# Kernel tuning notes

Hardware: AMD Instinct MI355X
Metric: run time of the kernel (lower is better)

## Reference

```python
import jax, jax.numpy as jnp
import numpy as np

RANK = 16
ALPHA = 32
SCALING = ALPHA / RANK  # 2.0


def setup_inputs() -> dict:
    key = jax.random.key(0)
    k1, k2, k3 = jax.random.split(key, 3)
    B_, S, D, O = 2, 4096, 4096, 4096
    x = jax.random.normal(k1, (B_, S, D), dtype=jnp.float32)
    # Dequantized base weight, torch Linear layout [out, in]
    W_base = jax.random.normal(k2, (O, D), dtype=jnp.float32) * 0.02
    # kaiming_uniform-ish init for lora_A [rank, in]
    bound = float(np.sqrt(6.0 / (1 + 5) / D))
    A = jax.random.uniform(k3, (RANK, D), dtype=jnp.float32, minval=-bound, maxval=bound)
    # lora_B initialized to zeros [out, rank]
    Bm = jnp.zeros((O, RANK), dtype=jnp.float32)
    return {"x": x, "W_base": W_base, "A": A, "B": Bm}


def reference(x, W_base, A, B):
    # Y = x @ W_base^T + (x @ A^T) @ B^T * scaling   (dropout p=0 -> identity)
    base_out = jnp.einsum('bsd,od->bso', x, W_base)
    lora_mid = jnp.einsum('bsd,rd->bsr', x, A)        # [B,S,rank]
    lora_out = jnp.einsum('bsr,or->bso', lora_mid, B) # [B,S,out]
    return base_out + lora_out * SCALING
```

## Files before the change

### kernel.cpp

```cpp
#include <hip/hip_runtime.h>
#include <hip/hip_bf16.h>

typedef __attribute__((ext_vector_type(8)))  __bf16 bf16x8;
typedef __attribute__((ext_vector_type(4)))  float  f32x4;

__global__ __launch_bounds__(256) void preproc(
    const float* __restrict__ x, const float* __restrict__ A,
    const float* __restrict__ Wf,
    float* __restrict__ mid, __bf16* __restrict__ Xb, __bf16* __restrict__ Wbb,
    int K, int M, long nW8, int wBlocks)
{
    int tid = threadIdx.x;
    if ((int)blockIdx.x < wBlocks) {
        long i = (long)blockIdx.x * 256 + tid;
        long stride = (long)wBlocks * 256;
        for (; i < nW8; i += stride) {
            const f32x4* p = (const f32x4*)(Wf + i * 8);
            f32x4 a = p[0], b = p[1];
            bf16x8 o;
            o[0] = (__bf16)a[0]; o[1] = (__bf16)a[1];
            o[2] = (__bf16)a[2]; o[3] = (__bf16)a[3];
            o[4] = (__bf16)b[0]; o[5] = (__bf16)b[1];
            o[6] = (__bf16)b[2]; o[7] = (__bf16)b[3];
            *(bf16x8*)(Wbb + i * 8) = o;
        }
        return;
    }

    int m0 = ((int)blockIdx.x - wBlocks) * 4;
    float acc[4][16];
#pragma unroll
    for (int row = 0; row < 4; ++row)
#pragma unroll
        for (int r = 0; r < 16; ++r) acc[row][r] = 0.f;

    int iters = K / 2048;
    for (int it = 0; it < iters; ++it) {
        int k = it * 2048 + tid * 8;
        f32x4 xv[4][2];
#pragma unroll
        for (int row = 0; row < 4; ++row) {
            if (m0 + row < M) {
                const float* xr = x + (size_t)(m0 + row) * K;
                xv[row][0] = *(const f32x4*)(xr + k);
                xv[row][1] = *(const f32x4*)(xr + k + 4);
                bf16x8 o;
                o[0] = (__bf16)xv[row][0][0]; o[1] = (__bf16)xv[row][0][1];
                o[2] = (__bf16)xv[row][0][2]; o[3] = (__bf16)xv[row][0][3];
                o[4] = (__bf16)xv[row][1][0]; o[5] = (__bf16)xv[row][1][1];
                o[6] = (__bf16)xv[row][1][2]; o[7] = (__bf16)xv[row][1][3];
                *(bf16x8*)(Xb + (size_t)(m0 + row) * K + k) = o;
            } else {
                f32x4 z = {0.f,0.f,0.f,0.f};
                xv[row][0] = z; xv[row][1] = z;
            }
        }
#pragma unroll
        for (int r = 0; r < 16; ++r) {
            const f32x4* ap = (const f32x4*)(A + (size_t)r * K + k);
            f32x4 a0 = ap[0], a1 = ap[1];
#pragma unroll
            for (int row = 0; row < 4; ++row) {
                acc[row][r] += xv[row][0][0]*a0[0] + xv[row][0][1]*a0[1]
                             + xv[row][0][2]*a0[2] + xv[row][0][3]*a0[3]
                             + xv[row][1][0]*a1[0] + xv[row][1][1]*a1[1]
                             + xv[row][1][2]*a1[2] + xv[row][1][3]*a1[3];
            }
        }
    }

#pragma unroll
    for (int row = 0; row < 4; ++row)
#pragma unroll
        for (int r = 0; r < 16; ++r)
#pragma unroll
            for (int off = 32; off > 0; off >>= 1)
                acc[row][r] += __shfl_down(acc[row][r], off, 64);

    __shared__ float red[4][4][16];
    int lane = tid & 63, w = tid >> 6;
    if (lane == 0) {
#pragma unroll
        for (int row = 0; row < 4; ++row)
#pragma unroll
            for (int r = 0; r < 16; ++r) red[w][row][r] = acc[row][r];
    }
    __syncthreads();
    if (tid < 64) {
        int row = tid >> 4, r = tid & 15;
        if (m0 + row < M) {
            float s = red[0][row][r] + red[1][row][r]
                    + red[2][row][r] + red[3][row][r];
            mid[(size_t)(m0 + row) * 16 + r] = s;
        }
    }
}

__global__ __launch_bounds__(256) void mid_only(
    const float* __restrict__ x, const float* __restrict__ A,
    float* __restrict__ mid, int K, int M)
{
    int tid = threadIdx.x;
    int m0 = blockIdx.x * 4;
    float acc[4][16];
#pragma unroll
    for (int row = 0; row < 4; ++row)
#pragma unroll
        for (int r = 0; r < 16; ++r) acc[row][r] = 0.f;
    int iters = K / 2048;
    for (int it = 0; it < iters; ++it) {
        int k = it * 2048 + tid * 8;
        f32x4 xv[4][2];
#pragma unroll
        for (int row = 0; row < 4; ++row) {
            if (m0 + row < M) {
                const float* xr = x + (size_t)(m0 + row) * K;
                xv[row][0] = *(const f32x4*)(xr + k);
                xv[row][1] = *(const f32x4*)(xr + k + 4);
            } else {
                f32x4 z = {0.f,0.f,0.f,0.f};
                xv[row][0] = z; xv[row][1] = z;
            }
        }
#pragma unroll
        for (int r = 0; r < 16; ++r) {
            const f32x4* ap = (const f32x4*)(A + (size_t)r * K + k);
            f32x4 a0 = ap[0], a1 = ap[1];
#pragma unroll
            for (int row = 0; row < 4; ++row) {
                acc[row][r] += xv[row][0][0]*a0[0] + xv[row][0][1]*a0[1]
                             + xv[row][0][2]*a0[2] + xv[row][0][3]*a0[3]
                             + xv[row][1][0]*a1[0] + xv[row][1][1]*a1[1]
                             + xv[row][1][2]*a1[2] + xv[row][1][3]*a1[3];
            }
        }
    }
#pragma unroll
    for (int row = 0; row < 4; ++row)
#pragma unroll
        for (int r = 0; r < 16; ++r)
#pragma unroll
            for (int off = 32; off > 0; off >>= 1)
                acc[row][r] += __shfl_down(acc[row][r], off, 64);
    __shared__ float red[4][4][16];
    int lane = tid & 63, w = tid >> 6;
    if (lane == 0) {
#pragma unroll
        for (int row = 0; row < 4; ++row)
#pragma unroll
            for (int r = 0; r < 16; ++r) red[w][row][r] = acc[row][r];
    }
    __syncthreads();
    if (tid < 64) {
        int row = tid >> 4, r = tid & 15;
        if (m0 + row < M) {
            float s = red[0][row][r] + red[1][row][r]
                    + red[2][row][r] + red[3][row][r];
            mid[(size_t)(m0 + row) * 16 + r] = s;
        }
    }
}

#define GL16(g, l) __builtin_amdgcn_global_load_lds( \
    (const __attribute__((address_space(1))) void*)(g), \
    (__attribute__((address_space(3))) void*)(l), 16, 0, 0)

#define DSR(dst, addr, IMM) \
    asm volatile("ds_read_b128 %0, %1 offset:" IMM : "=v"(dst) : "v"(addr))

#define BAR()   __builtin_amdgcn_s_barrier()
#define LGKM0() asm volatile("s_waitcnt lgkmcnt(0)" ::: )
#define FENCE() __builtin_amdgcn_sched_barrier(0)
#define VMW(n)  asm volatile("s_waitcnt vmcnt(" #n ")" ::: "memory")

__global__ __launch_bounds__(512, 2) void gemm256(
    const __bf16* __restrict__ Xb,
    const __bf16* __restrict__ Wb,
    const float*  __restrict__ mid,
    const float*  __restrict__ Bl,
    float* __restrict__ out,
    int M, int N, int K)
{
    __shared__ __bf16 As[4][256 * 32];
    __shared__ __bf16 Bs[4][256 * 32];

    const int NT = K >> 5;

    int nbx = N >> 8, nby = M >> 8, nwg = nbx * nby;
    int bid = blockIdx.x, swz = bid;
    if ((nwg & 7) == 0) { int cpx = nwg >> 3; swz = (bid & 7) * cpx + (bid >> 3); }
    int by = swz / nbx, bx = swz % nbx;
    int m0 = by << 8, n0 = bx << 8;

    int tid = threadIdx.x;
    int lane = tid & 63;
    int w = tid >> 6;
    int wm = w >> 2, wn = w & 3;

    int q0 = tid >> 2;
    int c0 = tid & 3;
    int csrc = c0 ^ ((q0 >> 1) & 3);
    const __bf16* sA0 = Xb + (size_t)(m0 + q0) * K + csrc * 8;
    const __bf16* sA1 = sA0 + (size_t)128 * K;
    const __bf16* sB0 = Wb + (size_t)(n0 + q0) * K + csrc * 8;
    const __bf16* sB1 = sB0 + (size_t)128 * K;
    unsigned ldsw = (unsigned)w * 1024;

#define STAGE_A(t, b) do { size_t ko = (size_t)(t) * 32; \
    GL16(sA0 + ko, (char*)As[b] + ldsw); \
    GL16(sA1 + ko, (char*)As[b] + 8192 + ldsw); } while (0)
#define STAGE_B(t, b) do { size_t ko = (size_t)(t) * 32; \
    GL16(sB0 + ko, (char*)Bs[b] + ldsw); \
    GL16(sB1 + ko, (char*)Bs[b] + 8192 + ldsw); } while (0)

    int chunkSwz = (lane >> 4) ^ ((lane >> 1) & 3);
    unsigned aoff = (unsigned)((wm * 128 + (lane & 15)) * 64 + chunkSwz * 16);
    unsigned boff = (unsigned)((wn * 64  + (lane & 15)) * 64 + chunkSwz * 16);
    unsigned a_addr = (unsigned)(size_t)(__attribute__((address_space(3))) __bf16*)&As[0][0] + aoff;
    unsigned b_addr = (unsigned)(size_t)(__attribute__((address_space(3))) __bf16*)&Bs[0][0] + boff;

    f32x4 acc[8][4];
    {
        int kh = lane >> 4;
        bf16x8 bI[4];
#pragma unroll
        for (int j = 0; j < 4; ++j) {
            bf16x8 v = {};
            if (kh < 2) {
                int col = n0 + wn * 64 + j * 16 + (lane & 15);
                const f32x4* p = (const f32x4*)(Bl + (size_t)col * 16 + kh * 8);
                f32x4 v0 = p[0], v1 = p[1];
                v[0] = (__bf16)(2.0f * v0[0]); v[1] = (__bf16)(2.0f * v0[1]);
                v[2] = (__bf16)(2.0f * v0[2]); v[3] = (__bf16)(2.0f * v0[3]);
                v[4] = (__bf16)(2.0f * v1[0]); v[5] = (__bf16)(2.0f * v1[1]);
                v[6] = (__bf16)(2.0f * v1[2]); v[7] = (__bf16)(2.0f * v1[3]);
            }
            bI[j] = v;
        }
#pragma unroll
        for (int i = 0; i < 8; ++i) {
            bf16x8 aI = {};
            if (kh < 2) {
                int row = m0 + wm * 128 + i * 16 + (lane & 15);
                const f32x4* p = (const f32x4*)(mid + (size_t)row * 16 + kh * 8);
                f32x4 v0 = p[0], v1 = p[1];
                aI[0] = (__bf16)v0[0]; aI[1] = (__bf16)v0[1];
                aI[2] = (__bf16)v0[2]; aI[3] = (__bf16)v0[3];
                aI[4] = (__bf16)v1[0]; aI[5] = (__bf16)v1[1];
                aI[6] = (__bf16)v1[2]; aI[7] = (__bf16)v1[3];
            }
            f32x4 z = {0.f, 0.f, 0.f, 0.f};
#pragma unroll
            for (int j = 0; j < 4; ++j)
                acc[i][j] = __builtin_amdgcn_mfma_f32_16x16x32_bf16(aI, bI[j], z, 0, 0, 0);
        }
    }

    STAGE_A(0, 0); STAGE_B(0, 0);
    STAGE_A(1, 1); STAGE_B(1, 1);
    VMW(4);
    BAR();

    bf16x8 af0, af1, af2, af3, af4, af5, af6, af7, bf0, bf1, bf2, bf3;

    for (int t = 0; t < NT; ++t) {
        unsigned aT = a_addr + ((unsigned)(t & 3) << 14);
        unsigned bT = b_addr + ((unsigned)(t & 3) << 14);
        bool p2 = (t + 2) < NT;

        DSR(bf0, bT, "0");    DSR(bf1, bT, "1024");
        DSR(bf2, bT, "2048"); DSR(bf3, bT, "3072");
        DSR(af0, aT, "0");    DSR(af1, aT, "1024");
        DSR(af2, aT, "2048"); DSR(af3, aT, "3072");
        if (p2) STAGE_A(t + 2, (t + 2) & 3);
        BAR();
        LGKM0();
        FENCE();
        __builtin_amdgcn_s_setprio(1);
        acc[0][0] = __builtin_amdgcn_mfma_f32_16x16x32_bf16(af0, bf0, acc[0][0], 0, 0, 0);
        acc[0][1] = __builtin_amdgcn_mfma_f32_16x16x32_bf16(af0, bf1, acc[0][1], 0, 0, 0);
        acc[0][2] = __builtin_amdgcn_mfma_f32_16x16x32_bf16(af0, bf2, acc[0][2], 0, 0, 0);
        acc[0][3] = __builtin_amdgcn_mfma_f32_16x16x32_bf16(af0, bf3, acc[0][3], 0, 0, 0);
        acc[1][0] = __builtin_amdgcn_mfma_f32_16x16x32_bf16(af1, bf0, acc[1][0], 0, 0, 0);
        acc[1][1] = __builtin_amdgcn_mfma_f32_16x16x32_bf16(af1, bf1, acc[1][1], 0, 0, 0);
        acc[1][2] = __builtin_amdgcn_mfma_f32_16x16x32_bf16(af1, bf2, acc[1][2], 0, 0, 0);
        acc[1][3] = __builtin_amdgcn_mfma_f32_16x16x32_bf16(af1, bf3, acc[1][3], 0, 0, 0);
        acc[2][0] = __builtin_amdgcn_mfma_f32_16x16x32_bf16(af2, bf0, acc[2][0], 0, 0, 0);
        acc[2][1] = __builtin_amdgcn_mfma_f32_16x16x32_bf16(af2, bf1, acc[2][1], 0, 0, 0);
        acc[2][2] = __builtin_amdgcn_mfma_f32_16x16x32_bf16(af2, bf2, acc[2][2], 0, 0, 0);
        acc[2][3] = __builtin_amdgcn_mfma_f32_16x16x32_bf16(af2, bf3, acc[2][3], 0, 0, 0);
        acc[3][0] = __builtin_amdgcn_mfma_f32_16x16x32_bf16(af3, bf0, acc[3][0], 0, 0, 0);
        acc[3][1] = __builtin_amdgcn_mfma_f32_16x16x32_bf16(af3, bf1, acc[3][1], 0, 0, 0);
        acc[3][2] = __builtin_amdgcn_mfma_f32_16x16x32_bf16(af3, bf2, acc[3][2], 0, 0, 0);
        acc[3][3] = __builtin_amdgcn_mfma_f32_16x16x32_bf16(af3, bf3, acc[3][3], 0, 0, 0);
        __builtin_amdgcn_s_setprio(0);
        BAR();

        DSR(af4, aT, "4096"); DSR(af5, aT, "5120");
        DSR(af6, aT, "6144"); DSR(af7, aT, "7168");
        if (p2) {
            STAGE_B(t + 2, (t + 2) & 3);
            VMW(4);
        } else {
            VMW(0);
        }
        BAR();
        LGKM0();
        FENCE();
        __builtin_amdgcn_s_setprio(1);
        acc[4][0] = __builtin_amdgcn_mfma_f32_16x16x32_bf16(af4, bf0, acc[4][0], 0, 0, 0);
        acc[4][1] = __builtin_amdgcn_mfma_f32_16x16x32_bf16(af4, bf1, acc[4][1], 0, 0, 0);
        acc[4][2] = __builtin_amdgcn_mfma_f32_16x16x32_bf16(af4, bf2, acc[4][2], 0, 0, 0);
        acc[4][3] = __builtin_amdgcn_mfma_f32_16x16x32_bf16(af4, bf3, acc[4][3], 0, 0, 0);
        acc[5][0] = __builtin_amdgcn_mfma_f32_16x16x32_bf16(af5, bf0, acc[5][0], 0, 0, 0);
        acc[5][1] = __builtin_amdgcn_mfma_f32_16x16x32_bf16(af5, bf1, acc[5][1], 0, 0, 0);
        acc[5][2] = __builtin_amdgcn_mfma_f32_16x16x32_bf16(af5, bf2, acc[5][2], 0, 0, 0);
        acc[5][3] = __builtin_amdgcn_mfma_f32_16x16x32_bf16(af5, bf3, acc[5][3], 0, 0, 0);
        acc[6][0] = __builtin_amdgcn_mfma_f32_16x16x32_bf16(af6, bf0, acc[6][0], 0, 0, 0);
        acc[6][1] = __builtin_amdgcn_mfma_f32_16x16x32_bf16(af6, bf1, acc[6][1], 0, 0, 0);
        acc[6][2] = __builtin_amdgcn_mfma_f32_16x16x32_bf16(af6, bf2, acc[6][2], 0, 0, 0);
        acc[6][3] = __builtin_amdgcn_mfma_f32_16x16x32_bf16(af6, bf3, acc[6][3], 0, 0, 0);
        acc[7][0] = __builtin_amdgcn_mfma_f32_16x16x32_bf16(af7, bf0, acc[7][0], 0, 0, 0);
        acc[7][1] = __builtin_amdgcn_mfma_f32_16x16x32_bf16(af7, bf1, acc[7][1], 0, 0, 0);
        acc[7][2] = __builtin_amdgcn_mfma_f32_16x16x32_bf16(af7, bf2, acc[7][2], 0, 0, 0);
        acc[7][3] = __builtin_amdgcn_mfma_f32_16x16x32_bf16(af7, bf3, acc[7][3], 0, 0, 0);
        __builtin_amdgcn_s_setprio(0);
        BAR();
    }

#pragma unroll
    for (int i = 0; i < 8; ++i) {
        int rbase = m0 + wm * 128 + i * 16 + ((lane >> 4) << 2);
#pragma unroll
        for (int q = 0; q < 4; ++q) {
            float* orow = out + (size_t)(rbase + q) * N;
            int colb = n0 + wn * 64 + (lane & 15);
            orow[colb]      = acc[i][0][q];
            orow[colb + 16] = acc[i][1][q];
            orow[colb + 32] = acc[i][2][q];
            orow[colb + 48] = acc[i][3][q];
        }
    }
}

__global__ __launch_bounds__(256) void gemm_fb(
    const float* __restrict__ X, const float* __restrict__ W,
    const float* __restrict__ mid, const float* __restrict__ Bl,
    float* __restrict__ out, int M, int N, int K)
{
    __shared__ float As[64][16];
    __shared__ float Bs[64][16];
    int nbx = N / 64;
    int bx = blockIdx.x % nbx, by = blockIdx.x / nbx;
    int m0 = by * 64, n0 = bx * 64;
    int tid = threadIdx.x;
    int tr = tid >> 4, tc = tid & 15;

    float acc[4][4] = {};
    for (int kt = 0; kt < K; kt += 16) {
#pragma unroll
        for (int s = 0; s < 4; ++s) {
            int c = s * 256 + tid;
            int row = c >> 4, kk = c & 15;
            As[row][kk] = X[(size_t)(m0 + row) * K + kt + kk];
            Bs[row][kk] = W[(size_t)(n0 + row) * K + kt + kk];
        }
        __syncthreads();
#pragma unroll
        for (int kk = 0; kk < 16; ++kk) {
            float av[4], bv[4];
#pragma unroll
            for (int i = 0; i < 4; ++i) { av[i] = As[tr*4+i][kk]; bv[i] = Bs[tc*4+i][kk]; }
#pragma unroll
            for (int i = 0; i < 4; ++i)
#pragma unroll
                for (int j = 0; j < 4; ++j) acc[i][j] += av[i] * bv[j];
        }
        __syncthreads();
    }
#pragma unroll
    for (int i = 0; i < 4; ++i) {
        int row = m0 + tr * 4 + i;
#pragma unroll
        for (int j = 0; j < 4; ++j) {
            int col = n0 + tc * 4 + j;
            float s = 0.f;
#pragma unroll
            for (int r = 0; r < 16; ++r)
                s += mid[(size_t)row * 16 + r] * Bl[(size_t)col * 16 + r];
            out[(size_t)row * N + col] = acc[i][j] + 2.0f * s;
        }
    }
}

extern "C" void kernel_launch(void* const* d_in, const int* in_sizes, int n_in,
                              void* d_out, int out_size, void* d_ws, size_t ws_size,
                              hipStream_t stream)
{
    const float* x   = (const float*)d_in[0];
    const float* Wf  = (const float*)d_in[1];
    const float* A   = (const float*)d_in[2];
    const float* Bl  = (const float*)d_in[3];
    float* out = (float*)d_out;

    int D = in_sizes[2] / 16;
    int O = in_sizes[3] / 16;
    long M = (long)in_sizes[0] / D;
    int K = D, N = O;

    size_t xb_bytes  = (size_t)M * K * 2;
    size_t wb_bytes  = (size_t)N * K * 2;
    size_t mid_bytes = (size_t)M * 16 * 4;

    bool shapes_ok = (M % 256 == 0) && (N % 256 == 0) && (K % 2048 == 0)
                     && (K / 32 >= 8);

    int midBlocks = (int)((M + 3) / 4);

    if (shapes_ok && ws_size >= xb_bytes + wb_bytes + mid_bytes) {
        __bf16* Xb  = (__bf16*)d_ws;
        __bf16* Wbb = (__bf16*)((char*)d_ws + xb_bytes);
        float*  mid = (float*)((char*)d_ws + xb_bytes + wb_bytes);

        const int wBlocks = 1024;
        long nW8 = (long)N * K / 8;
        preproc<<<wBlocks + midBlocks, 256, 0, stream>>>(
            x, A, Wf, mid, Xb, Wbb, K, (int)M, nW8, wBlocks);
        int nwg = (int)(M / 256) * (N / 256);
        gemm256<<<nwg, 512, 0, stream>>>(Xb, Wbb, mid, Bl, out, (int)M, N, K);
    } else {
        float* mid = (float*)d_ws;
        mid_only<<<midBlocks, 256, 0, stream>>>(x, A, mid, K, (int)M);
        int nwg = (int)(M / 64) * (N / 64);
        gemm_fb<<<nwg, 256, 0, stream>>>(x, Wf, mid, Bl, out, (int)M, N, K);
    }
}
```

Measured before the change: 338.5 us.

## Double-buffer LDS fragments in registers and use one barrier per k-step

The main GEMM loop is restructured to process two k-tiles per iteration. It keeps two register sets of A/B fragments, so the LDS reads for the next tile are issued before the current tile's 32 MFMAs run. The two half-step barriers per tile become one, and the A and B global-to-LDS stages for a future tile are issued together. This is meant to hide LDS read latency and cut barrier stalls, at the cost of doubling fragment registers, which could spill or lower occupancy under the 512x2 launch bound. The combined vmcnt wait after staging both A and B may also be stricter than before.

```diff
diff --git a/kernel.cpp b/kernel.cpp
--- a/kernel.cpp
+++ b/kernel.cpp
@@ -170,8 +170,31 @@
 
 #define BAR()   __builtin_amdgcn_s_barrier()
 #define LGKM0() asm volatile("s_waitcnt lgkmcnt(0)" ::: )
-#define FENCE() __builtin_amdgcn_sched_barrier(0)
+#define SCHED() __builtin_amdgcn_sched_barrier(0)
 #define VMW(n)  asm volatile("s_waitcnt vmcnt(" #n ")" ::: "memory")
+
+#define MM(i, j, AF, BF) \
+    acc[i][j] = __builtin_amdgcn_mfma_f32_16x16x32_bf16(AF, BF, acc[i][j], 0, 0, 0)
+
+#define MFMA_BLOCK(A0,A1,A2,A3,A4,A5,A6,A7,B0,B1,B2,B3) do { \
+    MM(0,0,A0,B0); MM(0,1,A0,B1); MM(0,2,A0,B2); MM(0,3,A0,B3); \
+    MM(1,0,A1,B0); MM(1,1,A1,B1); MM(1,2,A1,B2); MM(1,3,A1,B3); \
+    MM(2,0,A2,B0); MM(2,1,A2,B1); MM(2,2,A2,B2); MM(2,3,A2,B3); \
+    MM(3,0,A3,B0); MM(3,1,A3,B1); MM(3,2,A3,B2); MM(3,3,A3,B3); \
+    MM(4,0,A4,B0); MM(4,1,A4,B1); MM(4,2,A4,B2); MM(4,3,A4,B3); \
+    MM(5,0,A5,B0); MM(5,1,A5,B1); MM(5,2,A5,B2); MM(5,3,A5,B3); \
+    MM(6,0,A6,B0); MM(6,1,A6,B1); MM(6,2,A6,B2); MM(6,3,A6,B3); \
+    MM(7,0,A7,B0); MM(7,1,A7,B1); MM(7,2,A7,B2); MM(7,3,A7,B3); \
+    } while (0)
+
+#define DSR_SET(PA, PB, a0,a1,a2,a3,a4,a5,a6,a7, b0,b1,b2,b3) do { \
+    DSR(a0, PA, "0");    DSR(a1, PA, "1024"); \
+    DSR(a2, PA, "2048"); DSR(a3, PA, "3072"); \
+    DSR(b0, PB, "0");    DSR(b1, PB, "1024"); \
+    DSR(b2, PB, "2048"); DSR(b3, PB, "3072"); \
+    DSR(a4, PA, "4096"); DSR(a5, PA, "5120"); \
+    DSR(a6, PA, "6144"); DSR(a7, PA, "7168"); \
+    } while (0)
 
 __global__ __launch_bounds__(512, 2) void gemm256(
     const __bf16* __restrict__ Xb,
@@ -261,71 +284,47 @@
     VMW(4);
     BAR();
 
-    bf16x8 af0, af1, af2, af3, af4, af5, af6, af7, bf0, bf1, bf2, bf3;
-
-    for (int t = 0; t < NT; ++t) {
-        unsigned aT = a_addr + ((unsigned)(t & 3) << 14);
-        unsigned bT = b_addr + ((unsigned)(t & 3) << 14);
+    bf16x8 xa0, xa1, xa2, xa3, xa4, xa5, xa6, xa7, xb0, xb1, xb2, xb3;
+    bf16x8 ya0, ya1, ya2, ya3, ya4, ya5, ya6, ya7, yb0, yb1, yb2, yb3;
+
+    DSR_SET(a_addr, b_addr, xa0,xa1,xa2,xa3,xa4,xa5,xa6,xa7, xb0,xb1,xb2,xb3);
+
+    for (int t = 0; t < NT; t += 2) {
+        unsigned bY  = (unsigned)((t + 1) & 3) << 14;
+        unsigned bX2 = (unsigned)((t + 2) & 3) << 14;
+        bool p1 = (t + 1) < NT;
         bool p2 = (t + 2) < NT;
-
-        DSR(bf0, bT, "0");    DSR(bf1, bT, "1024");
-        DSR(bf2, bT, "2048"); DSR(bf3, bT, "3072");
-        DSR(af0, aT, "0");    DSR(af1, aT, "1024");
-        DSR(af2, aT, "2048"); DSR(af3, aT, "3072");
-        if (p2) STAGE_A(t + 2, (t + 2) & 3);
+        bool p3 = (t + 3) < NT;
+
+        if (p2) { STAGE_A(t + 2, (t + 2) & 3); STAGE_B(t + 2, (t + 2) & 3); VMW(4); }
+        else    { VMW(0); }
         BAR();
         LGKM0();
-        FENCE();
+        SCHED();
+        if (p1) {
+            unsigned pA = a_addr + bY, pB = b_addr + bY;
+            DSR_SET(pA, pB, ya0,ya1,ya2,ya3,ya4,ya5,ya6,ya7, yb0,yb1,yb2,yb3);
+        }
+        SCHED();
         __builtin_amdgcn_s_setprio(1);
-        acc[0][0] = __builtin_amdgcn_mfma_f32_16x16x32_bf16(af0, bf0, acc[0][0], 0, 0, 0);
-        acc[0][1] = __builtin_amdgcn_mfma_f32_16x16x32_bf16(af0, bf1, acc[0][1], 0, 0, 0);
-        acc[0][2] = __builtin_amdgcn_mfma_f32_16x16x32_bf16(af0, bf2, acc[0][2], 0, 0, 0);
-        acc[0][3] = __builtin_amdgcn_mfma_f32_16x16x32_bf16(af0, bf3, acc[0][3], 0, 0, 0);
-        acc[1][0] = __builtin_amdgcn_mfma_f32_16x16x32_bf16(af1, bf0, acc[1][0], 0, 0, 0);
-        acc[1][1] = __builtin_amdgcn_mfma_f32_16x16x32_bf16(af1, bf1, acc[1][1], 0, 0, 0);
-        acc[1][2] = __builtin_amdgcn_mfma_f32_16x16x32_bf16(af1, bf2, acc[1][2], 0, 0, 0);
-        acc[1][3] = __builtin_amdgcn_mfma_f32_16x16x32_bf16(af1, bf3, acc[1][3], 0, 0, 0);
-        acc[2][0] = __builtin_amdgcn_mfma_f32_16x16x32_bf16(af2, bf0, acc[2][0], 0, 0, 0);
-        acc[2][1] = __builtin_amdgcn_mfma_f32_16x16x32_bf16(af2, bf1, acc[2][1], 0, 0, 0);
-        acc[2][2] = __builtin_amdgcn_mfma_f32_16x16x32_bf16(af2, bf2, acc[2][2], 0, 0, 0);
-        acc[2][3] = __builtin_amdgcn_mfma_f32_16x16x32_bf16(af2, bf3, acc[2][3], 0, 0, 0);
-        acc[3][0] = __builtin_amdgcn_mfma_f32_16x16x32_bf16(af3, bf0, acc[3][0], 0, 0, 0);
-        acc[3][1] = __builtin_amdgcn_mfma_f32_16x16x32_bf16(af3, bf1, acc[3][1], 0, 0, 0);
-        acc[3][2] = __builtin_amdgcn_mfma_f32_16x16x32_bf16(af3, bf2, acc[3][2], 0, 0, 0);
-        acc[3][3] = __builtin_amdgcn_mfma_f32_16x16x32_bf16(af3, bf3, acc[3][3], 0, 0, 0);
+        MFMA_BLOCK(xa0,xa1,xa2,xa3,xa4,xa5,xa6,xa7, xb0,xb1,xb2,xb3);
         __builtin_amdgcn_s_setprio(0);
-        BAR();
-
-        DSR(af4, aT, "4096"); DSR(af5, aT, "5120");
-        DSR(af6, aT, "6144"); DSR(af7, aT, "7168");
-        if (p2) {
-            STAGE_B(t + 2, (t + 2) & 3);
-            VMW(4);
-        } else {
-            VMW(0);
-        }
-        BAR();
-        LGKM0();
-        FENCE();
-        __builtin_amdgcn_s_setprio(1);
-        acc[4][0] = __builtin_amdgcn_mfma_f32_16x16x32_bf16(af4, bf0, acc[4][0], 0, 0, 0);
-        acc[4][1] = __builtin_amdgcn_mfma_f32_16x16x32_bf16(af4, bf1, acc[4][1], 0, 0, 0);
-        acc[4][2] = __builtin_amdgcn_mfma_f32_16x16x32_bf16(af4, bf2, acc[4][2], 0, 0, 0);
-        acc[4][3] = __builtin_amdgcn_mfma_f32_16x16x32_bf16(af4, bf3, acc[4][3], 0, 0, 0);
-        acc[5][0] = __builtin_amdgcn_mfma_f32_16x16x32_bf16(af5, bf0, acc[5][0], 0, 0, 0);
-        acc[5][1] = __builtin_amdgcn_mfma_f32_16x16x32_bf16(af5, bf1, acc[5][1], 0, 0, 0);
-        acc[5][2] = __builtin_amdgcn_mfma_f32_16x16x32_bf16(af5, bf2, acc[5][2], 0, 0, 0);
-        acc[5][3] = __builtin_amdgcn_mfma_f32_16x16x32_bf16(af5, bf3, acc[5][3], 0, 0, 0);
-        acc[6][0] = __builtin_amdgcn_mfma_f32_16x16x32_bf16(af6, bf0, acc[6][0], 0, 0, 0);
-        acc[6][1] = __builtin_amdgcn_mfma_f32_16x16x32_bf16(af6, bf1, acc[6][1], 0, 0, 0);
-        acc[6][2] = __builtin_amdgcn_mfma_f32_16x16x32_bf16(af6, bf2, acc[6][2], 0, 0, 0);
-        acc[6][3] = __builtin_amdgcn_mfma_f32_16x16x32_bf16(af6, bf3, acc[6][3], 0, 0, 0);
-        acc[7][0] = __builtin_amdgcn_mfma_f32_16x16x32_bf16(af7, bf0, acc[7][0], 0, 0, 0);
-        acc[7][1] = __builtin_amdgcn_mfma_f32_16x16x32_bf16(af7, bf1, acc[7][1], 0, 0, 0);
-        acc[7][2] = __builtin_amdgcn_mfma_f32_16x16x32_bf16(af7, bf2, acc[7][2], 0, 0, 0);
-        acc[7][3] = __builtin_amdgcn_mfma_f32_16x16x32_bf16(af7, bf3, acc[7][3], 0, 0, 0);
-        __builtin_amdgcn_s_setprio(0);
-        BAR();
+
+        if (p1) {
+            if (p3) { STAGE_A(t + 3, (t + 3) & 3); STAGE_B(t + 3, (t + 3) & 3); VMW(4); }
+            else    { VMW(0); }
+            BAR();
+            LGKM0();
+            SCHED();
+            if (p2) {
+                unsigned pA = a_addr + bX2, pB = b_addr + bX2;
+                DSR_SET(pA, pB, xa0,xa1,xa2,xa3,xa4,xa5,xa6,xa7, xb0,xb1,xb2,xb3);
+            }
+            SCHED();
+            __builtin_amdgcn_s_setprio(1);
+            MFMA_BLOCK(ya0,ya1,ya2,ya3,ya4,ya5,ya6,ya7, yb0,yb1,yb2,yb3);
+            __builtin_amdgcn_s_setprio(0);
+        }
     }
 
 #pragma unroll
```

Result: faster. 330.3 us (-2.4%).

## Shrink GEMM tile to 256x128 with double buffering and higher occupancy

Applied to the files above, without the earlier changes.

Replaces the 256x256 block tile (8 waves, each computing 128x64) with a 256x128 tile where each wave computes 64x64, and targets 4 workgroups per CU instead of 2. The 4-stage LDS ring with prefetch distance 2 becomes a simple 2-stage double buffer. Each step issues one combined A+B stage and waits for all memory with vmcnt(0) before the barrier. The aim is to raise occupancy and cut accumulator and LDS pressure so more waves hide latency. The cost is lower arithmetic intensity per tile, more global traffic for X, and a shallower prefetch pipeline that can stall on memory.

```diff
diff --git a/kernel.cpp b/kernel.cpp
--- a/kernel.cpp
+++ b/kernel.cpp
@@ -170,10 +170,10 @@
 
 #define BAR()   __builtin_amdgcn_s_barrier()
 #define LGKM0() asm volatile("s_waitcnt lgkmcnt(0)" ::: )
-#define FENCE() __builtin_amdgcn_sched_barrier(0)
-#define VMW(n)  asm volatile("s_waitcnt vmcnt(" #n ")" ::: "memory")
-
-__global__ __launch_bounds__(512, 2) void gemm256(
+#define SCHED() __builtin_amdgcn_sched_barrier(0)
+#define VMW0()  asm volatile("s_waitcnt vmcnt(0)" ::: "memory")
+
+__global__ __launch_bounds__(512, 4) void gemm256x128(
     const __bf16* __restrict__ Xb,
     const __bf16* __restrict__ Wb,
     const float*  __restrict__ mid,
@@ -181,21 +181,21 @@
     float* __restrict__ out,
     int M, int N, int K)
 {
-    __shared__ __bf16 As[4][256 * 32];
-    __shared__ __bf16 Bs[4][256 * 32];
+    __shared__ __bf16 As[2][256 * 32];
+    __shared__ __bf16 Bs[2][128 * 32];
 
     const int NT = K >> 5;
 
-    int nbx = N >> 8, nby = M >> 8, nwg = nbx * nby;
+    int nbx = N >> 7, nby = M >> 8, nwg = nbx * nby;
     int bid = blockIdx.x, swz = bid;
     if ((nwg & 7) == 0) { int cpx = nwg >> 3; swz = (bid & 7) * cpx + (bid >> 3); }
     int by = swz / nbx, bx = swz % nbx;
-    int m0 = by << 8, n0 = bx << 8;
+    int m0 = by << 8, n0 = bx << 7;
 
     int tid = threadIdx.x;
     int lane = tid & 63;
     int w = tid >> 6;
-    int wm = w >> 2, wn = w & 3;
+    int wm = w >> 1, wn = w & 1;
 
     int q0 = tid >> 2;
     int c0 = tid & 3;
@@ -203,23 +203,20 @@
     const __bf16* sA0 = Xb + (size_t)(m0 + q0) * K + csrc * 8;
     const __bf16* sA1 = sA0 + (size_t)128 * K;
     const __bf16* sB0 = Wb + (size_t)(n0 + q0) * K + csrc * 8;
-    const __bf16* sB1 = sB0 + (size_t)128 * K;
     unsigned ldsw = (unsigned)w * 1024;
 
-#define STAGE_A(t, b) do { size_t ko = (size_t)(t) * 32; \
+#define STAGE(t, b) do { size_t ko = (size_t)(t) * 32; \
     GL16(sA0 + ko, (char*)As[b] + ldsw); \
-    GL16(sA1 + ko, (char*)As[b] + 8192 + ldsw); } while (0)
-#define STAGE_B(t, b) do { size_t ko = (size_t)(t) * 32; \
-    GL16(sB0 + ko, (char*)Bs[b] + ldsw); \
-    GL16(sB1 + ko, (char*)Bs[b] + 8192 + ldsw); } while (0)
+    GL16(sA1 + ko, (char*)As[b] + 8192 + ldsw); \
+    GL16(sB0 + ko, (char*)Bs[b] + ldsw); } while (0)
 
     int chunkSwz = (lane >> 4) ^ ((lane >> 1) & 3);
-    unsigned aoff = (unsigned)((wm * 128 + (lane & 15)) * 64 + chunkSwz * 16);
-    unsigned boff = (unsigned)((wn * 64  + (lane & 15)) * 64 + chunkSwz * 16);
+    unsigned aoff = (unsigned)((wm * 64 + (lane & 15)) * 64 + chunkSwz * 16);
+    unsigned boff = (unsigned)((wn * 64 + (lane & 15)) * 64 + chunkSwz * 16);
     unsigned a_addr = (unsigned)(size_t)(__attribute__((address_space(3))) __bf16*)&As[0][0] + aoff;
     unsigned b_addr = (unsigned)(size_t)(__attribute__((address_space(3))) __bf16*)&Bs[0][0] + boff;
 
-    f32x4 acc[8][4];
+    f32x4 acc[4][4];
     {
         int kh = lane >> 4;
         bf16x8 bI[4];
@@ -238,10 +235,10 @@
             bI[j] = v;
         }
 #pragma unroll
-        for (int i = 0; i < 8; ++i) {
+        for (int i = 0; i < 4; ++i) {
             bf16x8 aI = {};
             if (kh < 2) {
-                int row = m0 + wm * 128 + i * 16 + (lane & 15);
+                int row = m0 + wm * 64 + i * 16 + (lane & 15);
                 const f32x4* p = (const f32x4*)(mid + (size_t)row * 16 + kh * 8);
                 f32x4 v0 = p[0], v1 = p[1];
                 aI[0] = (__bf16)v0[0]; aI[1] = (__bf16)v0[1];
@@ -256,26 +253,25 @@
         }
     }
 
-    STAGE_A(0, 0); STAGE_B(0, 0);
-    STAGE_A(1, 1); STAGE_B(1, 1);
-    VMW(4);
+    STAGE(0, 0);
+    VMW0();
     BAR();
 
-    bf16x8 af0, af1, af2, af3, af4, af5, af6, af7, bf0, bf1, bf2, bf3;
+    bf16x8 af0, af1, af2, af3, bf0, bf1, bf2, bf3;
 
     for (int t = 0; t < NT; ++t) {
-        unsigned aT = a_addr + ((unsigned)(t & 3) << 14);
-        unsigned bT = b_addr + ((unsigned)(t & 3) << 14);
-        bool p2 = (t + 2) < NT;
-
+        unsigned aT = a_addr + ((unsigned)(t & 1) << 14);
+        unsigned bT = b_addr + ((unsigned)(t & 1) << 13);
+        bool p1 = (t + 1) < NT;
+
+        if (p1) STAGE(t + 1, (t + 1) & 1);
+
+        DSR(af0, aT, "0");    DSR(af1, aT, "1024");
+        DSR(af2, aT, "2048"); DSR(af3, aT, "3072");
         DSR(bf0, bT, "0");    DSR(bf1, bT, "1024");
         DSR(bf2, bT, "2048"); DSR(bf3, bT, "3072");
-        DSR(af0, aT, "0");    DSR(af1, aT, "1024");
-        DSR(af2, aT, "2048"); DSR(af3, aT, "3072");
-        if (p2) STAGE_A(t + 2, (t + 2) & 3);
-        BAR();
         LGKM0();
-        FENCE();
+        SCHED();
         __builtin_amdgcn_s_setprio(1);
         acc[0][0] = __builtin_amdgcn_mfma_f32_16x16x32_bf16(af0, bf0, acc[0][0], 0, 0, 0);
         acc[0][1] = __builtin_amdgcn_mfma_f32_16x16x32_bf16(af0, bf1, acc[0][1], 0, 0, 0);
@@ -294,43 +290,14 @@
         acc[3][2] = __builtin_amdgcn_mfma_f32_16x16x32_bf16(af3, bf2, acc[3][2], 0, 0, 0);
         acc[3][3] = __builtin_amdgcn_mfma_f32_16x16x32_bf16(af3, bf3, acc[3][3], 0, 0, 0);
         __builtin_amdgcn_s_setprio(0);
+
+        if (p1) VMW0();
         BAR();
-
-        DSR(af4, aT, "4096"); DSR(af5, aT, "5120");
-        DSR(af6, aT, "6144"); DSR(af7, aT, "7168");
-        if (p2) {
-            STAGE_B(t + 2, (t + 2) & 3);
-            VMW(4);
-        } else {
-            VMW(0);
-        }
-        BAR();
-        LGKM0();
-        FENCE();
-        __builtin_amdgcn_s_setprio(1);
-        acc[4][0] = __builtin_amdgcn_mfma_f32_16x16x32_bf16(af4, bf0, acc[4][0], 0, 0, 0);
-        acc[4][1] = __builtin_amdgcn_mfma_f32_16x16x32_bf16(af4, bf1, acc[4][1], 0, 0, 0);
-        acc[4][2] = __builtin_amdgcn_mfma_f32_16x16x32_bf16(af4, bf2, acc[4][2], 0, 0, 0);
-        acc[4][3] = __builtin_amdgcn_mfma_f32_16x16x32_bf16(af4, bf3, acc[4][3], 0, 0, 0);
-        acc[5][0] = __builtin_amdgcn_mfma_f32_16x16x32_bf16(af5, bf0, acc[5][0], 0, 0, 0);
-        acc[5][1] = __builtin_amdgcn_mfma_f32_16x16x32_bf16(af5, bf1, acc[5][1], 0, 0, 0);
-        acc[5][2] = __builtin_amdgcn_mfma_f32_16x16x32_bf16(af5, bf2, acc[5][2], 0, 0, 0);
-        acc[5][3] = __builtin_amdgcn_mfma_f32_16x16x32_bf16(af5, bf3, acc[5][3], 0, 0, 0);
-        acc[6][0] = __builtin_amdgcn_mfma_f32_16x16x32_bf16(af6, bf0, acc[6][0], 0, 0, 0);
-        acc[6][1] = __builtin_amdgcn_mfma_f32_16x16x32_bf16(af6, bf1, acc[6][1], 0, 0, 0);
-        acc[6][2] = __builtin_amdgcn_mfma_f32_16x16x32_bf16(af6, bf2, acc[6][2], 0, 0, 0);
-        acc[6][3] = __builtin_amdgcn_mfma_f32_16x16x32_bf16(af6, bf3, acc[6][3], 0, 0, 0);
-        acc[7][0] = __builtin_amdgcn_mfma_f32_16x16x32_bf16(af7, bf0, acc[7][0], 0, 0, 0);
-        acc[7][1] = __builtin_amdgcn_mfma_f32_16x16x32_bf16(af7, bf1, acc[7][1], 0, 0, 0);
-        acc[7][2] = __builtin_amdgcn_mfma_f32_16x16x32_bf16(af7, bf2, acc[7][2], 0, 0, 0);
-        acc[7][3] = __builtin_amdgcn_mfma_f32_16x16x32_bf16(af7, bf3, acc[7][3], 0, 0, 0);
-        __builtin_amdgcn_s_setprio(0);
-        BAR();
-    }
-
-#pragma unroll
-    for (int i = 0; i < 8; ++i) {
-        int rbase = m0 + wm * 128 + i * 16 + ((lane >> 4) << 2);
+    }
+
+#pragma unroll
+    for (int i = 0; i < 4; ++i) {
+        int rbase = m0 + wm * 64 + i * 16 + ((lane >> 4) << 2);
 #pragma unroll
         for (int q = 0; q < 4; ++q) {
             float* orow = out + (size_t)(rbase + q) * N;
@@ -412,7 +379,7 @@
     size_t wb_bytes  = (size_t)N * K * 2;
     size_t mid_bytes = (size_t)M * 16 * 4;
 
-    bool shapes_ok = (M % 256 == 0) && (N % 256 == 0) && (K % 2048 == 0)
+    bool shapes_ok = (M % 256 == 0) && (N % 128 == 0) && (K % 2048 == 0)
                      && (K / 32 >= 8);
 
     int midBlocks = (int)((M + 3) / 4);
@@ -426,8 +393,8 @@
         long nW8 = (long)N * K / 8;
         preproc<<<wBlocks + midBlocks, 256, 0, stream>>>(
             x, A, Wf, mid, Xb, Wbb, K, (int)M, nW8, wBlocks);
-        int nwg = (int)(M / 256) * (N / 256);
-        gemm256<<<nwg, 512, 0, stream>>>(Xb, Wbb, mid, Bl, out, (int)M, N, K);
+        int nwg = (int)(M / 256) * (N / 128);
+        gemm256x128<<<nwg, 512, 0, stream>>>(Xb, Wbb, mid, Bl, out, (int)M, N, K);
     } else {
         float* mid = (float*)d_ws;
         mid_only<<<midBlocks, 256, 0, stream>>>(x, A, mid, K, (int)M);
```

Result: slower. 354.5 us (+4.7%).
